# Optimization experiments

Measured on AMD Instinct MI355X. Metric: run time of the kernel, lower is better.

The kernel has to match this reference:

```python
import jax, jax.numpy as jnp
import numpy as np

D_MODEL = 1024
N_HEADS = 16
D_HEAD = D_MODEL // N_HEADS
WINDOW = 256


def setup_inputs() -> dict:
    key = jax.random.key(0)
    ks = jax.random.split(key, 9)
    x = jax.random.normal(ks[0], (1, 4096, D_MODEL), dtype=jnp.float32)
    s = 0.02
    params = {
        'q_w': jax.random.normal(ks[1], (D_MODEL, D_MODEL), jnp.float32) * s,
        'q_b': jax.random.normal(ks[2], (D_MODEL,), jnp.float32) * s,
        'k_w': jax.random.normal(ks[3], (D_MODEL, D_MODEL), jnp.float32) * s,
        'k_b': jax.random.normal(ks[4], (D_MODEL,), jnp.float32) * s,
        'v_w': jax.random.normal(ks[5], (D_MODEL, D_MODEL), jnp.float32) * s,
        'v_b': jax.random.normal(ks[6], (D_MODEL,), jnp.float32) * s,
        'o_w': jax.random.normal(ks[7], (D_MODEL, D_MODEL), jnp.float32) * s,
        'o_b': jax.random.normal(ks[8], (D_MODEL,), jnp.float32) * s,
    }
    return {'x': x, **params}


def reference(x, q_w, q_b, k_w, k_b, v_w, v_b, o_w, o_b):
    B, S, D = x.shape
    scale = jnp.sqrt(jnp.float32(D_HEAD))
    # torch nn.Linear: y = x @ W.T + b
    q = (x @ q_w.T + q_b).reshape(B, S, N_HEADS, D_HEAD).transpose(0, 2, 1, 3)
    k = (x @ k_w.T + k_b).reshape(B, S, N_HEADS, D_HEAD).transpose(0, 2, 1, 3)
    v = (x @ v_w.T + v_b).reshape(B, S, N_HEADS, D_HEAD).transpose(0, 2, 1, 3)
    scores = jnp.einsum('bhqd,bhkd->bhqk', q, k) / scale  # [B,H,S,S]
    idx = jnp.arange(S)
    row = idx[:, None]
    col = idx[None, :]
    masked = (col > row) | (row - col >= min(WINDOW, S))
    scores = jnp.where(masked[None, None], -jnp.inf, scores)
    attn = jax.nn.softmax(scores, axis=-1)
    attn = jnp.nan_to_num(attn, nan=0.0)
    out = jnp.einsum('bhqk,bhkd->bhqd', attn, v)
    out = out.transpose(0, 2, 1, 3).reshape(B, S, D)
    return out @ o_w.T + o_b
```

## Files before the change

kernel.cpp:

```cpp
#include <hip/hip_runtime.h>
#include <hip/hip_bf16.h>

typedef __attribute__((ext_vector_type(4))) float f32x4;
typedef __attribute__((ext_vector_type(16))) float f32x16;
typedef __attribute__((ext_vector_type(8))) short short8;
typedef __attribute__((ext_vector_type(4))) int i32x4;

#define S_LEN 4096
#define DM    1024
#define NH    16
#define DH    64
#define WIN   256

__device__ inline unsigned short f2b(float f) {
  unsigned int x = __float_as_uint(f);
  unsigned int r = (x + 0x7fffu + ((x >> 16) & 1u)) >> 16;
  return (unsigned short)r;
}

__device__ inline void gload_lds16(const void* g, void* l) {
  __builtin_amdgcn_global_load_lds(
      (const __attribute__((address_space(1))) void*)g,
      (__attribute__((address_space(3))) void*)l, 16, 0, 0);
}

__global__ __launch_bounds__(256) void cvt_all(
    const float* __restrict__ x,
    const float* __restrict__ qw, const float* __restrict__ kw,
    const float* __restrict__ vw, const float* __restrict__ ow,
    unsigned short* __restrict__ Xb, unsigned short* __restrict__ Wb)
{
  const int y = blockIdx.y;
  const float* src;
  unsigned short* dst;
  int n8;
  if (y == 0) { src = x; dst = Xb; n8 = (S_LEN * DM) / 8; }
  else {
    src = (y == 1) ? qw : (y == 2) ? kw : (y == 3) ? vw : ow;
    dst = Wb + (size_t)(y - 1) * DM * DM;
    n8 = (DM * DM) / 8;
  }
  const int i = blockIdx.x * 256 + threadIdx.x;
  if (i >= n8) return;
  const float4* s4 = (const float4*)src + (size_t)i * 2;
  float4 a = s4[0], b = s4[1];
  short8 v;
  v[0] = f2b(a.x); v[1] = f2b(a.y); v[2] = f2b(a.z); v[3] = f2b(a.w);
  v[4] = f2b(b.x); v[5] = f2b(b.y); v[6] = f2b(b.z); v[7] = f2b(b.w);
  *(short8*)(dst + (size_t)i * 8) = v;
}

#define PIPE_WAIT8  asm volatile("s_waitcnt vmcnt(8)" ::: "memory")
#define PIPE_WAIT7  asm volatile("s_waitcnt vmcnt(7)" ::: "memory")
#define PIPE_WAIT0  asm volatile("s_waitcnt vmcnt(0)" ::: "memory")
#define PIPE_BAR    do { __builtin_amdgcn_s_barrier(); __builtin_amdgcn_sched_barrier(0); } while (0)
#define PIPE_ENDBAR do { __builtin_amdgcn_sched_barrier(0); __builtin_amdgcn_s_barrier(); \
                         __builtin_amdgcn_sched_barrier(0); } while (0)

__global__ __launch_bounds__(512, 1) void gemm_qkv_fused(
    const unsigned short* __restrict__ A,
    const unsigned short* __restrict__ W,
    const float* __restrict__ bq, const float* __restrict__ bk, const float* __restrict__ bv,
    unsigned short* __restrict__ Qb)
{
  constexpr int BM = 256, BN = 192;
  constexpr int REGA = BM * 64;
  constexpr int BUF = REGA + BN * 64;
  __shared__ __align__(16) unsigned short LDS[2 * BUF];
  unsigned short* A0 = LDS;
  unsigned short* B0 = LDS + REGA;
  unsigned short* A1 = LDS + BUF;
  unsigned short* B1 = LDS + BUF + REGA;

  const int t = threadIdx.x;
  const int lane = t & 63, w = t >> 6;
  const int wm = w >> 2, wn = w & 3;
  const int lr = lane & 15, lg = lane >> 4;
  const int m0 = blockIdx.x * BM, n0 = blockIdx.y * BN;

  int sr[4], sc[4], sb[4];
#pragma unroll
  for (int i = 0; i < 4; ++i) {
    const int bo = (i * 512 + w * 64) * 16;
    const int o = bo + lane * 16;
    const int row = o >> 7, colb = o & 127;
    const int colp = colb ^ ((row & 3) << 4) ^ (((row >> 2) & 1) << 6);
    sr[i] = row; sc[i] = colp >> 1; sb[i] = bo >> 1;
  }

#define STAGE(e0, lA, lB)                                                           \
  do {                                                                              \
    _Pragma("unroll") for (int i = 0; i < 4; ++i)                                   \
      gload_lds16(A + (size_t)(m0 + sr[i]) * DM + (e0) + sc[i], (lA) + sb[i]);      \
    _Pragma("unroll") for (int i = 0; i < 3; ++i)                                   \
      gload_lds16(W + (size_t)(n0 + sr[i]) * DM + (e0) + sc[i], (lB) + sb[i]);      \
  } while (0)

  f32x4 acc[8][3];
#pragma unroll
  for (int m = 0; m < 8; ++m)
#pragma unroll
    for (int n = 0; n < 3; ++n) acc[m][n] = (f32x4){0.f, 0.f, 0.f, 0.f};

  const int xor6l = ((lr >> 2) & 1) << 6;
  const int xor45 = (lg << 4) ^ ((lr & 3) << 4);

#define COMPUTE(sAp, sBp)                                                           \
  do {                                                                              \
    _Pragma("unroll") for (int kk = 0; kk < 2; ++kk) {                              \
      const int coff = ((kk << 6) ^ xor6l) + xor45;                                 \
      short8 af[8], bf[3];                                                          \
      _Pragma("unroll") for (int m = 0; m < 8; ++m)                                 \
        af[m] = *(const short8*)((const char*)(sAp) + (wm * 128 + m * 16 + lr) * 128 + coff); \
      _Pragma("unroll") for (int n = 0; n < 3; ++n)                                 \
        bf[n] = *(const short8*)((const char*)(sBp) + (wn * 48 + n * 16 + lr) * 128 + coff); \
      _Pragma("unroll") for (int m = 0; m < 8; ++m)                                 \
        _Pragma("unroll") for (int n = 0; n < 3; ++n)                               \
          acc[m][n] = __builtin_amdgcn_mfma_f32_16x16x32_bf16(af[m], bf[n], acc[m][n], 0, 0, 0); \
    }                                                                               \
  } while (0)

  STAGE(0, A0, B0);
#pragma unroll 1
  for (int kt = 0; kt < 14; kt += 2) {
    STAGE((kt + 1) * 64, A1, B1);
    PIPE_WAIT7; PIPE_BAR;
    __builtin_amdgcn_s_setprio(1);
    COMPUTE(A0, B0);
    __builtin_amdgcn_s_setprio(0);
    PIPE_ENDBAR;
    STAGE((kt + 2) * 64, A0, B0);
    PIPE_WAIT7; PIPE_BAR;
    __builtin_amdgcn_s_setprio(1);
    COMPUTE(A1, B1);
    __builtin_amdgcn_s_setprio(0);
    PIPE_ENDBAR;
  }
  STAGE(15 * 64, A1, B1);
  PIPE_WAIT7; PIPE_BAR;
  __builtin_amdgcn_s_setprio(1);
  COMPUTE(A0, B0);
  __builtin_amdgcn_s_setprio(0);
  PIPE_ENDBAR;
  PIPE_WAIT0; PIPE_BAR;
  __builtin_amdgcn_s_setprio(1);
  COMPUTE(A1, B1);
  __builtin_amdgcn_s_setprio(0);

#undef STAGE
#undef COMPUTE

#pragma unroll
  for (int n = 0; n < 3; ++n) {
    const int gc = n0 + wn * 48 + n * 16 + lr;
    const int slice = gc >> 10, col = gc & 1023;
    const float* bp = (slice == 0) ? bq : (slice == 1) ? bk : bv;
    const float bv_ = bp[col];
    unsigned short* Obase = Qb + (size_t)slice * ((size_t)S_LEN * DM);
#pragma unroll
    for (int m = 0; m < 8; ++m) {
      const int gr0 = m0 + wm * 128 + m * 16 + lg * 4;
#pragma unroll
      for (int r = 0; r < 4; ++r)
        Obase[(size_t)(gr0 + r) * DM + col] = f2b(acc[m][n][r] + bv_);
    }
  }
}

__global__ __launch_bounds__(256, 1) void gemm_out(
    const unsigned short* __restrict__ A,
    const unsigned short* __restrict__ Bmat,
    const float* __restrict__ bias,
    float* __restrict__ Of)
{
  constexpr int REG = 128 * 64;
  __shared__ __align__(16) unsigned short LDS[4 * REG];
  unsigned short* A0 = LDS;
  unsigned short* A1 = LDS + REG;
  unsigned short* B0 = LDS + 2 * REG;
  unsigned short* B1 = LDS + 3 * REG;

  const int t = threadIdx.x;
  const int lane = t & 63, w = t >> 6;
  const int wm = w >> 1, wn = w & 1;
  const int lr = lane & 15, lg = lane >> 4;
  const int m0 = blockIdx.x * 128, n0 = blockIdx.y * 128;

  int sr[4], sc[4], sb[4];
#pragma unroll
  for (int i = 0; i < 4; ++i) {
    const int bo = (i * 256 + w * 64) * 16;
    const int o = bo + lane * 16;
    const int row = o >> 7, colb = o & 127;
    const int colp = colb ^ ((row & 3) << 4) ^ (((row >> 2) & 1) << 6);
    sr[i] = row; sc[i] = colp >> 1; sb[i] = bo >> 1;
  }

#define STAGE(e0, lA, lB)                                                           \
  do {                                                                              \
    _Pragma("unroll") for (int i = 0; i < 4; ++i) {                                 \
      gload_lds16(A + (size_t)(m0 + sr[i]) * DM + (e0) + sc[i], (lA) + sb[i]);      \
      gload_lds16(Bmat + (size_t)(n0 + sr[i]) * DM + (e0) + sc[i], (lB) + sb[i]);   \
    }                                                                               \
  } while (0)

  f32x4 acc[4][4];
#pragma unroll
  for (int m = 0; m < 4; ++m)
#pragma unroll
    for (int n = 0; n < 4; ++n) acc[m][n] = (f32x4){0.f, 0.f, 0.f, 0.f};

  const int xor6l = ((lr >> 2) & 1) << 6;
  const int xor45 = (lg << 4) ^ ((lr & 3) << 4);

#define COMPUTE(sAp, sBp)                                                           \
  do {                                                                              \
    _Pragma("unroll") for (int kk = 0; kk < 2; ++kk) {                              \
      const int coff = ((kk << 6) ^ xor6l) + xor45;                                 \
      short8 af[4], bf[4];                                                          \
      _Pragma("unroll") for (int m = 0; m < 4; ++m)                                 \
        af[m] = *(const short8*)((const char*)(sAp) + (wm * 64 + m * 16 + lr) * 128 + coff); \
      _Pragma("unroll") for (int n = 0; n < 4; ++n)                                 \
        bf[n] = *(const short8*)((const char*)(sBp) + (wn * 64 + n * 16 + lr) * 128 + coff); \
      _Pragma("unroll") for (int m = 0; m < 4; ++m)                                 \
        _Pragma("unroll") for (int n = 0; n < 4; ++n)                               \
          acc[m][n] = __builtin_amdgcn_mfma_f32_16x16x32_bf16(af[m], bf[n], acc[m][n], 0, 0, 0); \
    }                                                                               \
  } while (0)

  STAGE(0, A0, B0);
#pragma unroll 1
  for (int kt = 0; kt < 14; kt += 2) {
    STAGE((kt + 1) * 64, A1, B1);
    PIPE_WAIT8; PIPE_BAR;
    __builtin_amdgcn_s_setprio(1);
    COMPUTE(A0, B0);
    __builtin_amdgcn_s_setprio(0);
    PIPE_ENDBAR;
    STAGE((kt + 2) * 64, A0, B0);
    PIPE_WAIT8; PIPE_BAR;
    __builtin_amdgcn_s_setprio(1);
    COMPUTE(A1, B1);
    __builtin_amdgcn_s_setprio(0);
    PIPE_ENDBAR;
  }
  STAGE(15 * 64, A1, B1);
  PIPE_WAIT8; PIPE_BAR;
  __builtin_amdgcn_s_setprio(1);
  COMPUTE(A0, B0);
  __builtin_amdgcn_s_setprio(0);
  PIPE_ENDBAR;
  PIPE_WAIT0; PIPE_BAR;
  __builtin_amdgcn_s_setprio(1);
  COMPUTE(A1, B1);
  __builtin_amdgcn_s_setprio(0);

#undef STAGE
#undef COMPUTE

#pragma unroll
  for (int n = 0; n < 4; ++n) {
    const int gc = n0 + wn * 64 + n * 16 + lr;
    const float bv = bias[gc];
#pragma unroll
    for (int m = 0; m < 4; ++m) {
      const int gr0 = m0 + wm * 64 + m * 16 + lg * 4;
#pragma unroll
      for (int r = 0; r < 4; ++r)
        Of[(size_t)(gr0 + r) * DM + gc] = acc[m][n][r] + bv;
    }
  }
}

__global__ __launch_bounds__(256) void attn(
    const unsigned short* __restrict__ Q,
    const unsigned short* __restrict__ Km,
    const unsigned short* __restrict__ Vm,
    unsigned short* __restrict__ AO)
{
  const int warp = threadIdx.x >> 6;
  const int l = threadIdx.x & 63;
  const int qw0 = (blockIdx.x * 4 + warp) * 32;
  const int hD = blockIdx.y * DH;
  const int q = l & 31;
  const int hi = l >> 5;
  const int l31 = l & 31;
  const int vkey = (l & 15) * 2;
  const int vd0 = (l >> 4) * 16;

  __shared__ __align__(16) unsigned short VtS[4][2][64 * 40];
  unsigned short* vt0 = &VtS[warp][0][0];
  unsigned short* vt1 = &VtS[warp][1][0];

  short8 qf[4];
  {
    const unsigned short* qp = Q + (size_t)(qw0 + q) * DM + hD + hi * 8;
#pragma unroll
    for (int ks = 0; ks < 4; ++ks) qf[ks] = *(const short8*)(qp + ks * 16);
  }

  f32x16 o0{}, o1{};
  float lsum = 0.f;

  const int kb0 = (qw0 >= WIN) ? (qw0 - WIN) : 0;
  const int nch = (qw0 + 32 - kb0) >> 5;

  short8 kfA[4], vfA[4], kfB[4], vfB[4];

#define LOADKV(kb_, kf_, vf_)                                                    \
  do {                                                                           \
    const unsigned short* kp_ = Km + (size_t)((kb_) + l31) * DM + hD + hi * 8;   \
    (kf_)[0] = *(const short8*)kp_;                                              \
    (kf_)[1] = *(const short8*)(kp_ + 16);                                       \
    (kf_)[2] = *(const short8*)(kp_ + 32);                                       \
    (kf_)[3] = *(const short8*)(kp_ + 48);                                       \
    const unsigned short* vp_ = Vm + (size_t)((kb_) + vkey) * DM + hD + vd0;     \
    (vf_)[0] = *(const short8*)vp_;                                              \
    (vf_)[1] = *(const short8*)(vp_ + 8);                                        \
    (vf_)[2] = *(const short8*)(vp_ + DM);                                       \
    (vf_)[3] = *(const short8*)(vp_ + DM + 8);                                   \
  } while (0)

#define PROCESS(kb_, kf_, vf_, vt_)                                             \
  do {                                                                          \
    const int kbv = (kb_);                                                      \
    _Pragma("unroll") for (int j = 0; j < 16; ++j) {                            \
      unsigned int wv = (unsigned int)(unsigned short)(vf_)[j >> 3][j & 7]      \
          | ((unsigned int)(unsigned short)(vf_)[2 + (j >> 3)][j & 7] << 16);   \
      *(unsigned int*)((vt_) + (vd0 + j) * 40 + vkey) = wv;                     \
    }                                                                           \
    f32x16 s{};                                                                 \
    _Pragma("unroll") for (int ks = 0; ks < 4; ++ks)                            \
      s = __builtin_amdgcn_mfma_f32_32x32x16_bf16((kf_)[ks], qf[ks], s, 0, 0, 0); \
    float p[16];                                                                \
    const bool isEdge = (kbv >= qw0) || (kbv + WIN - 32 < qw0);                 \
    if (isEdge) {                                                               \
      _Pragma("unroll") for (int r = 0; r < 16; ++r) {                          \
        const int key = kbv + (r & 3) + 8 * (r >> 2) + 4 * hi;                  \
        const int qg = qw0 + q;                                                 \
        const bool valid = (key <= qg) && (qg - key < WIN);                     \
        p[r] = valid ? __expf(s[r] * 0.125f) : 0.f;                             \
        lsum += p[r];                                                           \
      }                                                                         \
    } else {                                                                    \
      _Pragma("unroll") for (int r = 0; r < 16; ++r) {                          \
        p[r] = __expf(s[r] * 0.125f);                                           \
        lsum += p[r];                                                           \
      }                                                                         \
    }                                                                           \
    unsigned int u[8];                                                          \
    _Pragma("unroll") for (int t2 = 0; t2 < 4; ++t2) {                          \
      __hip_bfloat162 h0_ = __float22bfloat162_rn(make_float2(p[4 * t2], p[4 * t2 + 1])); \
      __hip_bfloat162 h1_ = __float22bfloat162_rn(make_float2(p[4 * t2 + 2], p[4 * t2 + 3])); \
      u[2 * t2]     = *(unsigned int*)&h0_;                                     \
      u[2 * t2 + 1] = *(unsigned int*)&h1_;                                     \
    }                                                                           \
    const unsigned int sd0 = hi ? u[0] : u[2], sd1 = hi ? u[1] : u[3];          \
    const unsigned int rc0 = __shfl_xor(sd0, 32, 64), rc1 = __shfl_xor(sd1, 32, 64); \
    const unsigned int sd2 = hi ? u[4] : u[6], sd3 = hi ? u[5] : u[7];          \
    const unsigned int rc2 = __shfl_xor(sd2, 32, 64), rc3 = __shfl_xor(sd3, 32, 64); \
    i32x4 pw0, pw1;                                                             \
    pw0[0] = hi ? rc0 : u[0]; pw0[1] = hi ? rc1 : u[1];                         \
    pw0[2] = hi ? u[2] : rc0; pw0[3] = hi ? u[3] : rc1;                         \
    pw1[0] = hi ? rc2 : u[4]; pw1[1] = hi ? rc3 : u[5];                         \
    pw1[2] = hi ? u[6] : rc2; pw1[3] = hi ? u[7] : rc3;                         \
    const short8 pf0 = *(const short8*)&pw0;                                    \
    const short8 pf1 = *(const short8*)&pw1;                                    \
    const short8 a00 = *(const short8*)((vt_) + l31 * 40 + hi * 8);             \
    const short8 a01 = *(const short8*)((vt_) + l31 * 40 + 16 + hi * 8);        \
    const short8 a10 = *(const short8*)((vt_) + (32 + l31) * 40 + hi * 8);      \
    const short8 a11 = *(const short8*)((vt_) + (32 + l31) * 40 + 16 + hi * 8); \
    o0 = __builtin_amdgcn_mfma_f32_32x32x16_bf16(a00, pf0, o0, 0, 0, 0);        \
    o0 = __builtin_amdgcn_mfma_f32_32x32x16_bf16(a01, pf1, o0, 0, 0, 0);        \
    o1 = __builtin_amdgcn_mfma_f32_32x32x16_bf16(a10, pf0, o1, 0, 0, 0);        \
    o1 = __builtin_amdgcn_mfma_f32_32x32x16_bf16(a11, pf1, o1, 0, 0, 0);        \
  } while (0)

  LOADKV(kb0, kfA, vfA);
  int c = 0;
#pragma unroll 1
  for (; c + 2 <= nch; c += 2) {
    const int kb = kb0 + c * 32;
    LOADKV(kb + 32, kfB, vfB);
    PROCESS(kb, kfA, vfA, vt0);
    if (c + 2 < nch) LOADKV(kb + 64, kfA, vfA);
    PROCESS(kb + 32, kfB, vfB, vt1);
  }
  if (c < nch) PROCESS(kb0 + c * 32, kfA, vfA, vt0);

#undef LOADKV
#undef PROCESS

  lsum += __shfl_xor(lsum, 32, 64);
  const float inv = 1.f / lsum;
  unsigned short* aop = AO + (size_t)(qw0 + q) * DM + hD;
#pragma unroll
  for (int t2 = 0; t2 < 4; ++t2) {
    __hip_bfloat162 s0 = __float22bfloat162_rn(make_float2(o0[4*t2] * inv, o0[4*t2+1] * inv));
    __hip_bfloat162 s1 = __float22bfloat162_rn(make_float2(o0[4*t2+2] * inv, o0[4*t2+3] * inv));
    uint2 st; st.x = *(unsigned int*)&s0; st.y = *(unsigned int*)&s1;
    *(uint2*)(aop + 8 * t2 + 4 * hi) = st;
    __hip_bfloat162 s2 = __float22bfloat162_rn(make_float2(o1[4*t2] * inv, o1[4*t2+1] * inv));
    __hip_bfloat162 s3 = __float22bfloat162_rn(make_float2(o1[4*t2+2] * inv, o1[4*t2+3] * inv));
    uint2 st2; st2.x = *(unsigned int*)&s2; st2.y = *(unsigned int*)&s3;
    *(uint2*)(aop + 32 + 8 * t2 + 4 * hi) = st2;
  }
}

extern "C" void kernel_launch(void* const* d_in, const int* in_sizes, int n_in,
                              void* d_out, int out_size, void* d_ws, size_t ws_size,
                              hipStream_t stream) {
  const float* x  = (const float*)d_in[0];
  const float* qw = (const float*)d_in[1];
  const float* qb = (const float*)d_in[2];
  const float* kw = (const float*)d_in[3];
  const float* kb = (const float*)d_in[4];
  const float* vw = (const float*)d_in[5];
  const float* vb = (const float*)d_in[6];
  const float* ow = (const float*)d_in[7];
  const float* ob = (const float*)d_in[8];

  const size_t SD = (size_t)S_LEN * DM;
  unsigned short* Qb  = (unsigned short*)d_ws;
  unsigned short* Kb  = Qb + SD;
  unsigned short* Vb  = Kb + SD;
  unsigned short* AOb = Vb + SD;
  unsigned short* Xb  = AOb + SD;
  unsigned short* Wcv = Xb + SD;

  cvt_all<<<dim3(2048, 5), 256, 0, stream>>>(x, qw, kw, vw, ow, Xb, Wcv);
  gemm_qkv_fused<<<dim3(16, 16), 512, 0, stream>>>(Xb, Wcv, qb, kb, vb, Qb);
  attn<<<dim3(S_LEN / 128, NH), 256, 0, stream>>>(Qb, Kb, Vb, AOb);
  gemm_out<<<dim3(32, 8), 256, 0, stream>>>(AOb, Wcv + (size_t)3 * DM * DM, ob, (float*)d_out);
}
```

Before: 81.58 us.

## Process two 32-query tiles per warp to share K/V loads

```diff
diff --git a/kernel.cpp b/kernel.cpp
--- a/kernel.cpp
+++ b/kernel.cpp
@@ -280,7 +280,7 @@
 {
   const int warp = threadIdx.x >> 6;
   const int l = threadIdx.x & 63;
-  const int qw0 = (blockIdx.x * 4 + warp) * 32;
+  const int qw0 = (blockIdx.x * 4 + warp) * 64;
   const int hD = blockIdx.y * DH;
   const int q = l & 31;
   const int hi = l >> 5;
@@ -292,20 +292,23 @@
   unsigned short* vt0 = &VtS[warp][0][0];
   unsigned short* vt1 = &VtS[warp][1][0];
 
-  short8 qf[4];
+  short8 qfA[4], qfB[4];
   {
     const unsigned short* qp = Q + (size_t)(qw0 + q) * DM + hD + hi * 8;
 #pragma unroll
-    for (int ks = 0; ks < 4; ++ks) qf[ks] = *(const short8*)(qp + ks * 16);
-  }
-
-  f32x16 o0{}, o1{};
-  float lsum = 0.f;
+    for (int ks = 0; ks < 4; ++ks) qfA[ks] = *(const short8*)(qp + ks * 16);
+    const unsigned short* qp2 = Q + (size_t)(qw0 + 32 + q) * DM + hD + hi * 8;
+#pragma unroll
+    for (int ks = 0; ks < 4; ++ks) qfB[ks] = *(const short8*)(qp2 + ks * 16);
+  }
+
+  f32x16 o0A{}, o1A{}, o0B{}, o1B{};
+  float lsumA = 0.f, lsumB = 0.f;
 
   const int kb0 = (qw0 >= WIN) ? (qw0 - WIN) : 0;
-  const int nch = (qw0 + 32 - kb0) >> 5;
-
-  short8 kfA[4], vfA[4], kfB[4], vfB[4];
+  const int nch = (qw0 + 64 - kb0) >> 5;
+
+  short8 kf1[4], vf1[4], kf2[4], vf2[4];
 
 #define LOADKV(kb_, kf_, vf_)                                                    \
   do {                                                                           \
@@ -321,31 +324,25 @@
     (vf_)[3] = *(const short8*)(vp_ + DM + 8);                                   \
   } while (0)
 
-#define PROCESS(kb_, kf_, vf_, vt_)                                             \
+#define TILE(qb_, qf_, o0_, o1_, ls_, kbv_, kf_, vt_)                           \
   do {                                                                          \
-    const int kbv = (kb_);                                                      \
-    _Pragma("unroll") for (int j = 0; j < 16; ++j) {                            \
-      unsigned int wv = (unsigned int)(unsigned short)(vf_)[j >> 3][j & 7]      \
-          | ((unsigned int)(unsigned short)(vf_)[2 + (j >> 3)][j & 7] << 16);   \
-      *(unsigned int*)((vt_) + (vd0 + j) * 40 + vkey) = wv;                     \
-    }                                                                           \
     f32x16 s{};                                                                 \
     _Pragma("unroll") for (int ks = 0; ks < 4; ++ks)                            \
-      s = __builtin_amdgcn_mfma_f32_32x32x16_bf16((kf_)[ks], qf[ks], s, 0, 0, 0); \
+      s = __builtin_amdgcn_mfma_f32_32x32x16_bf16((kf_)[ks], (qf_)[ks], s, 0, 0, 0); \
     float p[16];                                                                \
-    const bool isEdge = (kbv >= qw0) || (kbv + WIN - 32 < qw0);                 \
+    const bool isEdge = ((kbv_) >= (qb_)) || ((kbv_) + WIN - 32 < (qb_));       \
     if (isEdge) {                                                               \
       _Pragma("unroll") for (int r = 0; r < 16; ++r) {                          \
-        const int key = kbv + (r & 3) + 8 * (r >> 2) + 4 * hi;                  \
-        const int qg = qw0 + q;                                                 \
+        const int key = (kbv_) + (r & 3) + 8 * (r >> 2) + 4 * hi;               \
+        const int qg = (qb_) + q;                                               \
         const bool valid = (key <= qg) && (qg - key < WIN);                     \
         p[r] = valid ? __expf(s[r] * 0.125f) : 0.f;                             \
-        lsum += p[r];                                                           \
+        (ls_) += p[r];                                                          \
       }                                                                         \
     } else {                                                                    \
       _Pragma("unroll") for (int r = 0; r < 16; ++r) {                          \
         p[r] = __expf(s[r] * 0.125f);                                           \
-        lsum += p[r];                                                           \
+        (ls_) += p[r];                                                          \
       }                                                                         \
     }                                                                           \
     unsigned int u[8];                                                          \
@@ -370,40 +367,66 @@
     const short8 a01 = *(const short8*)((vt_) + l31 * 40 + 16 + hi * 8);        \
     const short8 a10 = *(const short8*)((vt_) + (32 + l31) * 40 + hi * 8);      \
     const short8 a11 = *(const short8*)((vt_) + (32 + l31) * 40 + 16 + hi * 8); \
-    o0 = __builtin_amdgcn_mfma_f32_32x32x16_bf16(a00, pf0, o0, 0, 0, 0);        \
-    o0 = __builtin_amdgcn_mfma_f32_32x32x16_bf16(a01, pf1, o0, 0, 0, 0);        \
-    o1 = __builtin_amdgcn_mfma_f32_32x32x16_bf16(a10, pf0, o1, 0, 0, 0);        \
-    o1 = __builtin_amdgcn_mfma_f32_32x32x16_bf16(a11, pf1, o1, 0, 0, 0);        \
-  } while (0)
-
-  LOADKV(kb0, kfA, vfA);
+    (o0_) = __builtin_amdgcn_mfma_f32_32x32x16_bf16(a00, pf0, (o0_), 0, 0, 0);  \
+    (o0_) = __builtin_amdgcn_mfma_f32_32x32x16_bf16(a01, pf1, (o0_), 0, 0, 0);  \
+    (o1_) = __builtin_amdgcn_mfma_f32_32x32x16_bf16(a10, pf0, (o1_), 0, 0, 0);  \
+    (o1_) = __builtin_amdgcn_mfma_f32_32x32x16_bf16(a11, pf1, (o1_), 0, 0, 0);  \
+  } while (0)
+
+#define CHUNK(kb_, kf_, vf_, vt_)                                               \
+  do {                                                                          \
+    const int kbC = (kb_);                                                      \
+    _Pragma("unroll") for (int j = 0; j < 16; ++j) {                            \
+      unsigned int wv = (unsigned int)(unsigned short)(vf_)[j >> 3][j & 7]      \
+          | ((unsigned int)(unsigned short)(vf_)[2 + (j >> 3)][j & 7] << 16);   \
+      *(unsigned int*)((vt_) + (vd0 + j) * 40 + vkey) = wv;                     \
+    }                                                                           \
+    if (kbC < qw0 + 32)                                                         \
+      TILE(qw0, qfA, o0A, o1A, lsumA, kbC, kf_, vt_);                           \
+    if (kbC >= qw0 - 254)                                                       \
+      TILE(qw0 + 32, qfB, o0B, o1B, lsumB, kbC, kf_, vt_);                      \
+  } while (0)
+
+  LOADKV(kb0, kf1, vf1);
   int c = 0;
 #pragma unroll 1
   for (; c + 2 <= nch; c += 2) {
     const int kb = kb0 + c * 32;
-    LOADKV(kb + 32, kfB, vfB);
-    PROCESS(kb, kfA, vfA, vt0);
-    if (c + 2 < nch) LOADKV(kb + 64, kfA, vfA);
-    PROCESS(kb + 32, kfB, vfB, vt1);
-  }
-  if (c < nch) PROCESS(kb0 + c * 32, kfA, vfA, vt0);
+    LOADKV(kb + 32, kf2, vf2);
+    CHUNK(kb, kf1, vf1, vt0);
+    if (c + 2 < nch) LOADKV(kb + 64, kf1, vf1);
+    CHUNK(kb + 32, kf2, vf2, vt1);
+  }
+  if (c < nch) CHUNK(kb0 + c * 32, kf1, vf1, vt0);
 
 #undef LOADKV
-#undef PROCESS
-
-  lsum += __shfl_xor(lsum, 32, 64);
-  const float inv = 1.f / lsum;
-  unsigned short* aop = AO + (size_t)(qw0 + q) * DM + hD;
+#undef TILE
+#undef CHUNK
+
+  lsumA += __shfl_xor(lsumA, 32, 64);
+  lsumB += __shfl_xor(lsumB, 32, 64);
+  const float invA = 1.f / lsumA;
+  const float invB = 1.f / lsumB;
+  unsigned short* aopA = AO + (size_t)(qw0 + q) * DM + hD;
+  unsigned short* aopB = AO + (size_t)(qw0 + 32 + q) * DM + hD;
 #pragma unroll
   for (int t2 = 0; t2 < 4; ++t2) {
-    __hip_bfloat162 s0 = __float22bfloat162_rn(make_float2(o0[4*t2] * inv, o0[4*t2+1] * inv));
-    __hip_bfloat162 s1 = __float22bfloat162_rn(make_float2(o0[4*t2+2] * inv, o0[4*t2+3] * inv));
+    __hip_bfloat162 s0 = __float22bfloat162_rn(make_float2(o0A[4*t2] * invA, o0A[4*t2+1] * invA));
+    __hip_bfloat162 s1 = __float22bfloat162_rn(make_float2(o0A[4*t2+2] * invA, o0A[4*t2+3] * invA));
     uint2 st; st.x = *(unsigned int*)&s0; st.y = *(unsigned int*)&s1;
-    *(uint2*)(aop + 8 * t2 + 4 * hi) = st;
-    __hip_bfloat162 s2 = __float22bfloat162_rn(make_float2(o1[4*t2] * inv, o1[4*t2+1] * inv));
-    __hip_bfloat162 s3 = __float22bfloat162_rn(make_float2(o1[4*t2+2] * inv, o1[4*t2+3] * inv));
+    *(uint2*)(aopA + 8 * t2 + 4 * hi) = st;
+    __hip_bfloat162 s2 = __float22bfloat162_rn(make_float2(o1A[4*t2] * invA, o1A[4*t2+1] * invA));
+    __hip_bfloat162 s3 = __float22bfloat162_rn(make_float2(o1A[4*t2+2] * invA, o1A[4*t2+3] * invA));
     uint2 st2; st2.x = *(unsigned int*)&s2; st2.y = *(unsigned int*)&s3;
-    *(uint2*)(aop + 32 + 8 * t2 + 4 * hi) = st2;
+    *(uint2*)(aopA + 32 + 8 * t2 + 4 * hi) = st2;
+    __hip_bfloat162 s4 = __float22bfloat162_rn(make_float2(o0B[4*t2] * invB, o0B[4*t2+1] * invB));
+    __hip_bfloat162 s5 = __float22bfloat162_rn(make_float2(o0B[4*t2+2] * invB, o0B[4*t2+3] * invB));
+    uint2 st3; st3.x = *(unsigned int*)&s4; st3.y = *(unsigned int*)&s5;
+    *(uint2*)(aopB + 8 * t2 + 4 * hi) = st3;
+    __hip_bfloat162 s6 = __float22bfloat162_rn(make_float2(o1B[4*t2] * invB, o1B[4*t2+1] * invB));
+    __hip_bfloat162 s7 = __float22bfloat162_rn(make_float2(o1B[4*t2+2] * invB, o1B[4*t2+3] * invB));
+    uint2 st4; st4.x = *(unsigned int*)&s6; st4.y = *(unsigned int*)&s7;
+    *(uint2*)(aopB + 32 + 8 * t2 + 4 * hi) = st4;
   }
 }
 
@@ -430,6 +453,6 @@
 
   cvt_all<<<dim3(2048, 5), 256, 0, stream>>>(x, qw, kw, vw, ow, Xb, Wcv);
   gemm_qkv_fused<<<dim3(16, 16), 512, 0, stream>>>(Xb, Wcv, qb, kb, vb, Qb);
-  attn<<<dim3(S_LEN / 128, NH), 256, 0, stream>>>(Qb, Kb, Vb, AOb);
+  attn<<<dim3(S_LEN / 256, NH), 256, 0, stream>>>(Qb, Kb, Vb, AOb);
   gemm_out<<<dim3(32, 8), 256, 0, stream>>>(AOb, Wcv + (size_t)3 * DM * DM, ob, (float*)d_out);
 }
```

Measured after the change: 79.55 us. 1.03x faster.
